# Kernel optimization log

Hardware: AMD Instinct MI355X
Metric: run time of the kernel (lower is better)

## Reference

```python
import jax, jax.numpy as jnp
import numpy as np
import math

EMBED_DIM = 768
NUM_HEADS = 12
HEAD_DIM = EMBED_DIM // NUM_HEADS
R = 16
LORA_ALPHA = 16
SCALING = LORA_ALPHA / math.sqrt(R)  # 4.0
U = 1.0  # ramp_up_steps=0 -> u()=1.0


def lora_linear(x, W, b, A):
    # base F.linear + SingLoRA delta: delta_W = A @ A.T (symmetric)
    base = x @ W.T + b
    delta_W = A @ A.T  # [D, D]
    return base + (x @ delta_W.T) * (U * SCALING)


def setup_inputs() -> dict:
    key = jax.random.key(0)
    ks = jax.random.split(key, 16)
    B, S, D = 2, 2048, EMBED_DIM
    inv = 1.0 / math.sqrt(D)
    d = {
        'query': jax.random.normal(ks[0], (B, S, D), jnp.float32),
        'key': jax.random.normal(ks[1], (B, S, D), jnp.float32),
        'value': jax.random.normal(ks[2], (B, S, D), jnp.float32),
        'Wq': jax.random.normal(ks[3], (D, D), jnp.float32) * inv,
        'bq': jax.random.normal(ks[4], (D,), jnp.float32) * 0.01,
        'Aq': jax.random.normal(ks[5], (D, R), jnp.float32) * 0.01,
        'Wk': jax.random.normal(ks[6], (D, D), jnp.float32) * inv,
        'bk': jax.random.normal(ks[7], (D,), jnp.float32) * 0.01,
        'Ak': jax.random.normal(ks[8], (D, R), jnp.float32) * 0.01,
        'Wv': jax.random.normal(ks[9], (D, D), jnp.float32) * inv,
        'bv': jax.random.normal(ks[10], (D,), jnp.float32) * 0.01,
        'Av': jax.random.normal(ks[11], (D, R), jnp.float32) * 0.01,
        'Wo': jax.random.normal(ks[12], (D, D), jnp.float32) * inv,
        'bo': jax.random.normal(ks[13], (D,), jnp.float32) * 0.01,
    }
    return d


def reference(query, key, value, Wq, bq, Aq, Wk, bk, Ak, Wv, bv, Av, Wo, bo):
    B, S, D = query.shape
    H, hd = NUM_HEADS, HEAD_DIM
    q = lora_linear(query, Wq, bq, Aq)
    k = lora_linear(key, Wk, bk, Ak)
    v = lora_linear(value, Wv, bv, Av)
    # [B, S, D] -> [B, H, S, hd]
    q = q.reshape(B, S, H, hd).transpose(0, 2, 1, 3)
    k = k.reshape(B, S, H, hd).transpose(0, 2, 1, 3)
    v = v.reshape(B, S, H, hd).transpose(0, 2, 1, 3)
    scores = jnp.einsum('bhqd,bhkd->bhqk', q, k) / math.sqrt(hd)
    attn = jax.nn.softmax(scores, axis=-1)
    out = jnp.einsum('bhqk,bhkd->bhqd', attn, v)  # [B, H, S, hd]
    out = out.transpose(0, 2, 1, 3).reshape(B, S, D)
    out = out @ Wo.T + bo
    return out
```

## Files before the change

kernel.cpp:

```cpp
#include <hip/hip_runtime.h>
#include <math.h>
#include <stdint.h>

#define D 768
#define S 2048
#define B_ 2
#define NROWS 4096
#define H 12
#define HD 64
#define R_ 16

typedef _Float16 half_t;
typedef _Float16 half8 __attribute__((ext_vector_type(8)));
typedef _Float16 half4 __attribute__((ext_vector_type(4)));
typedef float floatx4 __attribute__((ext_vector_type(4)));

#define MFMA32(a, b, c) __builtin_amdgcn_mfma_f32_16x16x32_f16(a, b, c, 0, 0, 0)
#define MFMA16(a, b, c) __builtin_amdgcn_mfma_f32_16x16x16f16(a, b, c, 0, 0, 0)
#define EXP2F(x) __builtin_amdgcn_exp2f(x)

__device__ __forceinline__ void gl_lds16(const void* gp, half_t* lp) {
  __builtin_amdgcn_global_load_lds(
      (const __attribute__((address_space(1))) void*)(gp),
      (__attribute__((address_space(3))) void*)(lp), 16, 0, 0);
}

__global__ __launch_bounds__(256) void build_M4_kernel(
    const float* __restrict__ Wq, const float* __restrict__ Aq,
    const float* __restrict__ Wk, const float* __restrict__ Ak,
    const float* __restrict__ Wv, const float* __restrict__ Av,
    const float* __restrict__ Wo, half_t* __restrict__ Mq,
    half_t* __restrict__ Mk, half_t* __restrict__ Mv,
    half_t* __restrict__ Mo) {
  const int y = blockIdx.y;
  const float* W = (y == 0) ? Wq : (y == 1) ? Wk : (y == 2) ? Wv : Wo;
  const float* A = (y == 0) ? Aq : (y == 1) ? Ak : (y == 2) ? Av : nullptr;
  half_t* M = (y == 0) ? Mq : (y == 1) ? Mk : (y == 2) ? Mv : Mo;
  int idx = blockIdx.x * 256 + threadIdx.x;
  int j = idx / D;
  int kk = idx - j * D;
  float acc = W[idx];
  if (A != nullptr) {
    float s = 0.f;
#pragma unroll
    for (int r = 0; r < R_; ++r) s += A[kk * R_ + r] * A[j * R_ + r];
    acc += 4.0f * s;
  }
  M[idx] = (half_t)acc;
}

__global__ __launch_bounds__(256) void gemm_qkv_kernel(
    const float* __restrict__ x0, const float* __restrict__ x1,
    const float* __restrict__ x2, const half_t* __restrict__ m0,
    const half_t* __restrict__ m1, const half_t* __restrict__ m2,
    const float* __restrict__ b0, const float* __restrict__ b1,
    const float* __restrict__ b2, half_t* __restrict__ o0,
    half_t* __restrict__ o1, half_t* __restrict__ o2) {
  constexpr int PB = 32 * 512;
  constexpr int TRS = 136;
  __shared__ __align__(16) half_t smem[2 * PB];

  const int z = blockIdx.z;
  const float* X = (z == 0) ? x0 : (z == 1) ? x1 : x2;
  const half_t* M = (z == 0) ? m0 : (z == 1) ? m1 : m2;
  const float* bias = (z == 0) ? b0 : (z == 1) ? b1 : b2;
  half_t* Out = (z == 0) ? o0 : (z == 1) ? o1 : o2;

  const int tid = threadIdx.x;
  const int lane = tid & 63;
  const int wv = tid >> 6;
  const int lr = lane & 15;
  const int lq = lane >> 4;
  const int row0 = blockIdx.y * 128;
  const int j0 = blockIdx.x * 128;
  const int wr = wv >> 1;
  const int wc = wv & 1;

  const int g_ = tid >> 4;
  const int a_ = tid & 15;
  const int arow0 = row0 + (g_ >> 1) * 16 + (a_ & 3) * 4;
  const int acolb = (g_ & 1) * 32 + (a_ >> 2) * 8;

  floatx4 acc[4][4] = {};
  float4 ra[8];

#define LOADA(k0)                                                              \
  do {                                                                         \
    _Pragma("unroll") for (int i = 0; i < 4; ++i) {                            \
      const float* p = X + (size_t)(arow0 + i) * D + (k0) + acolb;             \
      ra[2 * i] = *reinterpret_cast<const float4*>(p);                         \
      ra[2 * i + 1] = *reinterpret_cast<const float4*>(p + 4);                 \
    }                                                                          \
  } while (0)

#define WRITEA(bufi)                                                           \
  do {                                                                         \
    _Pragma("unroll") for (int i = 0; i < 4; ++i) {                            \
      half8 hh;                                                                \
      hh[0] = (half_t)ra[2 * i].x;                                             \
      hh[1] = (half_t)ra[2 * i].y;                                             \
      hh[2] = (half_t)ra[2 * i].z;                                             \
      hh[3] = (half_t)ra[2 * i].w;                                             \
      hh[4] = (half_t)ra[2 * i + 1].x;                                         \
      hh[5] = (half_t)ra[2 * i + 1].y;                                         \
      hh[6] = (half_t)ra[2 * i + 1].z;                                         \
      hh[7] = (half_t)ra[2 * i + 1].w;                                         \
      *reinterpret_cast<half8*>(smem + (bufi)*PB + 32 * tid + 8 * i) = hh;     \
    }                                                                          \
  } while (0)

#define STAGEB(bufi, k0)                                                       \
  do {                                                                         \
    _Pragma("unroll") for (int gi = 0; gi < 4; ++gi) {                         \
      int gb = wv * 4 + gi;                                                    \
      int u = gb >> 1, cb = gb & 1;                                            \
      gl_lds16(M + (size_t)(j0 + u * 16 + lr) * D + (k0) + cb * 32 + lq * 8,   \
               smem + (bufi)*PB + 16 * 512 + gb * 512);                        \
    }                                                                          \
  } while (0)

  STAGEB(0, 0);
  LOADA(0);
  WRITEA(0);
  __syncthreads();

  for (int it = 0; it < D / 64; ++it) {
    const int cur = it & 1;
    if (it + 1 < D / 64) {
      STAGEB(cur ^ 1, (it + 1) * 64);
      LOADA((it + 1) * 64);
    }
    const half_t* Ab = smem + cur * PB;
    const half_t* Bb = Ab + 16 * 512;
#pragma unroll
    for (int c = 0; c < 2; ++c) {
      half8 af[4], bf[4];
#pragma unroll
      for (int t = 0; t < 4; ++t)
        af[t] = *reinterpret_cast<const half8*>(
            &Ab[(((wr * 4 + t) * 2 + c) * 64 + lane) * 8]);
#pragma unroll
      for (int u = 0; u < 4; ++u)
        bf[u] = *reinterpret_cast<const half8*>(
            &Bb[(((wc * 4 + u) * 2 + c) * 64 + lane) * 8]);
#pragma unroll
      for (int t = 0; t < 4; ++t)
#pragma unroll
        for (int u = 0; u < 4; ++u) acc[t][u] = MFMA32(af[t], bf[u], acc[t][u]);
    }
    if (it + 1 < D / 64) WRITEA(cur ^ 1);
    __syncthreads();
  }
#undef LOADA
#undef WRITEA
#undef STAGEB

  float bv[4];
#pragma unroll
  for (int u = 0; u < 4; ++u) bv[u] = bias[j0 + (wc * 4 + u) * 16 + lr];

  if (z == 2) {
#pragma unroll
    for (int t = 0; t < 4; ++t) {
#pragma unroll
      for (int u = 0; u < 4; ++u) {
        int c_local = (wc * 4 + u) * 16 + lr;
#pragma unroll
        for (int r = 0; r < 4; ++r) {
          int r_local = (wr * 4 + t) * 16 + lq * 4 + r;
          smem[c_local * TRS + r_local] = (half_t)(acc[t][u][r] + bv[u]);
        }
      }
    }
    __syncthreads();
    const int bb = row0 >> 11;
    const int s_base = row0 & 2047;
#pragma unroll
    for (int it = 0; it < 8; ++it) {
      int unit = it * 256 + tid;
      int c_local = unit >> 4;
      int chunk = unit & 15;
      half8 vv =
          *reinterpret_cast<const half8*>(&smem[c_local * TRS + chunk * 8]);
      int gc = j0 + c_local;
      int hh = gc >> 6, dd = gc & 63;
      *reinterpret_cast<half8*>(
          &Out[((size_t)(bb * H + hh) * HD + dd) * S + s_base + chunk * 8]) = vv;
    }
    return;
  }

#pragma unroll
  for (int t = 0; t < 4; ++t) {
#pragma unroll
    for (int u = 0; u < 4; ++u) {
#pragma unroll
      for (int r = 0; r < 4; ++r) {
        int gr = row0 + (wr * 4 + t) * 16 + lq * 4 + r;
        int gc = j0 + (wc * 4 + u) * 16 + lr;
        Out[(size_t)gr * D + gc] = (half_t)(acc[t][u][r] + bv[u]);
      }
    }
  }
}

__global__ __launch_bounds__(256) void gemm_o_kernel(
    const half_t* __restrict__ Xh, const half_t* __restrict__ M,
    const float* __restrict__ bias, float* __restrict__ Out) {
  constexpr int AG = 8;
  constexpr int G = AG + 16;
  constexpr int PB = G * 512;
  __shared__ __align__(16) half_t smem[2 * PB];

  const int tid = threadIdx.x;
  const int lane = tid & 63;
  const int wv = tid >> 6;
  const int lr = lane & 15;
  const int lq = lane >> 4;
  const int row0 = blockIdx.y * 64;
  const int j0 = blockIdx.x * 128;
  const int wc = wv;

  floatx4 acc[4][2] = {};

#define GSTAGE(bufi, k0)                                                       \
  do {                                                                         \
    _Pragma("unroll") for (int gi = 0; gi < 6; ++gi) {                         \
      int g = wv * 6 + gi;                                                     \
      if (g < AG) {                                                            \
        int t = g >> 1, c = g & 1;                                             \
        gl_lds16(                                                              \
            Xh + (size_t)(row0 + t * 16 + lr) * D + (k0) + c * 32 + lq * 8,    \
            smem + (bufi)*PB + g * 512);                                       \
      } else {                                                                 \
        int g2 = g - AG;                                                       \
        int u = g2 >> 1, c = g2 & 1;                                           \
        gl_lds16(                                                              \
            M + (size_t)(j0 + u * 16 + lr) * D + (k0) + c * 32 + lq * 8,       \
            smem + (bufi)*PB + AG * 512 + g2 * 512);                           \
      }                                                                        \
    }                                                                          \
  } while (0)

  GSTAGE(0, 0);
  __syncthreads();

  for (int it = 0; it < D / 64; ++it) {
    const int cur = it & 1;
    if (it + 1 < D / 64) GSTAGE(cur ^ 1, (it + 1) * 64);
    const half_t* Ab = smem + cur * PB;
    const half_t* Bb = Ab + AG * 512;
#pragma unroll
    for (int c = 0; c < 2; ++c) {
      half8 af[4], bf[2];
#pragma unroll
      for (int t = 0; t < 4; ++t)
        af[t] = *reinterpret_cast<const half8*>(
            &Ab[((t * 2 + c) * 64 + lane) * 8]);
#pragma unroll
      for (int u = 0; u < 2; ++u)
        bf[u] = *reinterpret_cast<const half8*>(
            &Bb[(((wc * 2 + u) * 2 + c) * 64 + lane) * 8]);
#pragma unroll
      for (int t = 0; t < 4; ++t)
#pragma unroll
        for (int u = 0; u < 2; ++u) acc[t][u] = MFMA32(af[t], bf[u], acc[t][u]);
    }
    __syncthreads();
  }
#undef GSTAGE

  float bv[2];
#pragma unroll
  for (int u = 0; u < 2; ++u) bv[u] = bias[j0 + (wc * 2 + u) * 16 + lr];
#pragma unroll
  for (int t = 0; t < 4; ++t) {
#pragma unroll
    for (int u = 0; u < 2; ++u) {
#pragma unroll
      for (int r = 0; r < 4; ++r) {
        int gr = row0 + t * 16 + lq * 4 + r;
        int gc = j0 + (wc * 2 + u) * 16 + lr;
        Out[(size_t)gr * D + gc] = acc[t][u][r] + bv[u];
      }
    }
  }
}

__global__ __launch_bounds__(512, 6) void attn_mfma_kernel(
    const half_t* __restrict__ Qh, const half_t* __restrict__ Kh,
    const half_t* __restrict__ Vt_g, half_t* __restrict__ Oh) {
  __shared__ __align__(16) half_t smem[16384];
  half_t* Ks = smem;
  half_t* Vs = smem + 8192;

  const int tid = threadIdx.x;
  const int lane = tid & 63;
  const int wv = tid >> 6;
  const int t_ = wv & 3;
  const int half_ = wv >> 2;
  const int lr = lane & 15;
  const int lq = lane >> 4;
  const int q0 = blockIdx.x * 64;
  const int h = blockIdx.y;
  const int b = blockIdx.z;
  const size_t base = (size_t)b * S * D + h * HD;
  const size_t vtbase = (size_t)(b * H + h) * HD * (size_t)S;
  const int qw = q0 + t_ * 16;

  const half_t qscale = (half_t)0.18033688f;
  half8 qf[2];
#pragma unroll
  for (int c = 0; c < 2; ++c) {
    half8 qv = *reinterpret_cast<const half8*>(
        &Qh[base + (size_t)(qw + lr) * D + c * 32 + lq * 8]);
#pragma unroll
    for (int j = 0; j < 8; ++j) qv[j] = qv[j] * qscale;
    qf[c] = qv;
  }

  half4 ones;
#pragma unroll
  for (int j = 0; j < 4; ++j) ones[j] = (half_t)1.0f;

  floatx4 o[4] = {};
  floatx4 ol = {};

#define STAGE(bufi, kb)                                                        \
  do {                                                                         \
    _Pragma("unroll") for (int gi = 0; gi < 2; ++gi) {                         \
      int g = wv * 2 + gi;                                                     \
      if (g < 8) {                                                             \
        int u = g >> 1, c = g & 1;                                             \
        gl_lds16(                                                              \
            Kh + base + (size_t)((kb) + u * 16 + lr) * D + c * 32 + lq * 8,    \
            Ks + (bufi)*4096 + g * 512);                                       \
      } else {                                                                 \
        int gv = g - 8;                                                        \
        int ud = gv >> 1, c = gv & 1;                                          \
        gl_lds16(                                                              \
            Vt_g + vtbase + (size_t)(ud * 16 + lr) * S + (kb) + c * 32 +       \
                lq * 8,                                                        \
            Vs + (bufi)*4096 + gv * 512);                                      \
      }                                                                        \
    }                                                                          \
  } while (0)

  STAGE(0, 0);
  __syncthreads();

  for (int it = 0; it < S / 64; ++it) {
    const int cur = it & 1;
    if (it + 1 < S / 64) STAGE(cur ^ 1, (it + 1) * 64);

#pragma unroll
    for (int ui = 0; ui < 2; ++ui) {
      const int u = half_ * 2 + ui;
      half8 kf0 = *reinterpret_cast<const half8*>(
          &Ks[cur * 4096 + ((u * 2 + 0) * 64 + lane) * 8]);
      half8 kf1 = *reinterpret_cast<const half8*>(
          &Ks[cur * 4096 + ((u * 2 + 1) * 64 + lane) * 8]);
      floatx4 st = {};
      st = MFMA32(kf0, qf[0], st);
      st = MFMA32(kf1, qf[1], st);
      half4 pf;
      pf[0] = (half_t)EXP2F(st[0]);
      pf[1] = (half_t)EXP2F(st[1]);
      pf[2] = (half_t)EXP2F(st[2]);
      pf[3] = (half_t)EXP2F(st[3]);
#pragma unroll
      for (int ud = 0; ud < 4; ++ud) {
        half4 vf = *reinterpret_cast<const half4*>(
            &Vs[cur * 4096 + ((ud * 2 + (u >> 1)) * 64 +
                              ((((u & 1) * 2) + (lq >> 1)) * 16 + lr)) *
                                 8 +
                (lq & 1) * 4]);
        o[ud] = MFMA16(pf, vf, o[ud]);
      }
      ol = MFMA16(pf, ones, ol);
    }
    __syncthreads();
  }
#undef STAGE

  float* red = (float*)smem;
  const int slot = t_ * 64 + lane;
  if (half_ == 1) {
#pragma unroll
    for (int comp = 0; comp < 16; ++comp)
      red[comp * 260 + slot] = o[comp >> 2][comp & 3];
#pragma unroll
    for (int r = 0; r < 4; ++r) red[(16 + r) * 260 + slot] = ol[r];
  }
  __syncthreads();
  if (half_ == 0) {
#pragma unroll
    for (int comp = 0; comp < 16; ++comp)
      o[comp >> 2][comp & 3] += red[comp * 260 + slot];
    float linv[4];
#pragma unroll
    for (int r = 0; r < 4; ++r)
      linv[r] = 1.0f / (ol[r] + red[(16 + r) * 260 + slot]);
#pragma unroll
    for (int ud = 0; ud < 4; ++ud) {
#pragma unroll
      for (int r = 0; r < 4; ++r) {
        int row = qw + lq * 4 + r;
        int col = h * HD + ud * 16 + lr;
        Oh[(size_t)(b * S + row) * D + col] = (half_t)(o[ud][r] * linv[r]);
      }
    }
  }
}

extern "C" void kernel_launch(void* const* d_in, const int* in_sizes, int n_in,
                              void* d_out, int out_size, void* d_ws,
                              size_t ws_size, hipStream_t stream) {
  const float* query = (const float*)d_in[0];
  const float* key   = (const float*)d_in[1];
  const float* value = (const float*)d_in[2];
  const float* Wq = (const float*)d_in[3];
  const float* bq = (const float*)d_in[4];
  const float* Aq = (const float*)d_in[5];
  const float* Wk = (const float*)d_in[6];
  const float* bk = (const float*)d_in[7];
  const float* Ak = (const float*)d_in[8];
  const float* Wv = (const float*)d_in[9];
  const float* bv = (const float*)d_in[10];
  const float* Av = (const float*)d_in[11];
  const float* Wo = (const float*)d_in[12];
  const float* bo = (const float*)d_in[13];
  float* out = (float*)d_out;

  half_t* hw = (half_t*)d_ws;
  const size_t XSZ = (size_t)NROWS * D;
  const size_t MSZ = (size_t)D * D;
  half_t* qh = hw;
  half_t* kh = qh + XSZ;
  half_t* vt = kh + XSZ;
  half_t* ab = vt + XSZ;
  half_t* Mq = ab + XSZ;
  half_t* Mk = Mq + MSZ;
  half_t* Mv = Mk + MSZ;
  half_t* Mo = Mv + MSZ;

  dim3 gm(D * D / 256, 4);
  build_M4_kernel<<<gm, 256, 0, stream>>>(Wq, Aq, Wk, Ak, Wv, Av, Wo, Mq, Mk,
                                          Mv, Mo);

  dim3 gq(D / 128, NROWS / 128, 3);
  gemm_qkv_kernel<<<gq, 256, 0, stream>>>(query, key, value, Mq, Mk, Mv, bq,
                                          bk, bv, qh, kh, vt);

  dim3 ga(S / 64, H, B_);
  attn_mfma_kernel<<<ga, 512, 0, stream>>>(qh, kh, vt, ab);

  dim3 go(D / 128, NROWS / 64, 1);
  gemm_o_kernel<<<go, 256, 0, stream>>>(ab, Mo, bo, out);
}
```

Measured before the change: 243.5 us.

## Pre-convert QKV inputs to fp16 and stage GEMM operands via direct LDS loads

```diff
diff --git a/kernel.cpp b/kernel.cpp
--- a/kernel.cpp
+++ b/kernel.cpp
@@ -25,43 +25,60 @@
       (__attribute__((address_space(3))) void*)(lp), 16, 0, 0);
 }
 
-__global__ __launch_bounds__(256) void build_M4_kernel(
+__global__ __launch_bounds__(256) void prep_kernel(
+    const float* __restrict__ q, const float* __restrict__ k,
+    const float* __restrict__ v, half_t* __restrict__ xq,
+    half_t* __restrict__ xk, half_t* __restrict__ xv,
     const float* __restrict__ Wq, const float* __restrict__ Aq,
     const float* __restrict__ Wk, const float* __restrict__ Ak,
     const float* __restrict__ Wv, const float* __restrict__ Av,
     const float* __restrict__ Wo, half_t* __restrict__ Mq,
     half_t* __restrict__ Mk, half_t* __restrict__ Mv,
     half_t* __restrict__ Mo) {
-  const int y = blockIdx.y;
-  const float* W = (y == 0) ? Wq : (y == 1) ? Wk : (y == 2) ? Wv : Wo;
-  const float* A = (y == 0) ? Aq : (y == 1) ? Ak : (y == 2) ? Av : nullptr;
-  half_t* M = (y == 0) ? Mq : (y == 1) ? Mk : (y == 2) ? Mv : Mo;
-  int idx = blockIdx.x * 256 + threadIdx.x;
-  int j = idx / D;
-  int kk = idx - j * D;
-  float acc = W[idx];
-  if (A != nullptr) {
-    float s = 0.f;
-#pragma unroll
-    for (int r = 0; r < R_; ++r) s += A[kk * R_ + r] * A[j * R_ + r];
-    acc += 4.0f * s;
-  }
-  M[idx] = (half_t)acc;
+  const int bid = blockIdx.x;
+  if (bid < 9216) {
+    const int y = bid / 3072;
+    const float* x = (y == 0) ? q : (y == 1) ? k : v;
+    half_t* o = (y == 0) ? xq : (y == 1) ? xk : xv;
+    int i = (bid - y * 3072) * 1024 + threadIdx.x * 4;
+    float4 vv = *reinterpret_cast<const float4*>(x + i);
+    half_t tmp[4] = {(half_t)vv.x, (half_t)vv.y, (half_t)vv.z, (half_t)vv.w};
+    *reinterpret_cast<uint64_t*>(o + i) = *reinterpret_cast<uint64_t*>(tmp);
+  } else {
+    const int u = bid - 9216;
+    const int y = u / 2304;
+    const float* W = (y == 0) ? Wq : (y == 1) ? Wk : (y == 2) ? Wv : Wo;
+    const float* A = (y == 0) ? Aq : (y == 1) ? Ak : (y == 2) ? Av : nullptr;
+    half_t* M = (y == 0) ? Mq : (y == 1) ? Mk : (y == 2) ? Mv : Mo;
+    int idx = (u - y * 2304) * 256 + threadIdx.x;
+    int j = idx / D;
+    int kk = idx - j * D;
+    float acc = W[idx];
+    if (A != nullptr) {
+      float s = 0.f;
+#pragma unroll
+      for (int r = 0; r < R_; ++r) s += A[kk * R_ + r] * A[j * R_ + r];
+      acc += 4.0f * s;
+    }
+    M[idx] = (half_t)acc;
+  }
 }
 
 __global__ __launch_bounds__(256) void gemm_qkv_kernel(
-    const float* __restrict__ x0, const float* __restrict__ x1,
-    const float* __restrict__ x2, const half_t* __restrict__ m0,
+    const half_t* __restrict__ x0, const half_t* __restrict__ x1,
+    const half_t* __restrict__ x2, const half_t* __restrict__ m0,
     const half_t* __restrict__ m1, const half_t* __restrict__ m2,
     const float* __restrict__ b0, const float* __restrict__ b1,
     const float* __restrict__ b2, half_t* __restrict__ o0,
     half_t* __restrict__ o1, half_t* __restrict__ o2) {
-  constexpr int PB = 32 * 512;
-  constexpr int TRS = 136;
+  constexpr int AG = 8;
+  constexpr int G = AG + 16;
+  constexpr int PB = G * 512;
+  constexpr int TRS = 72;
   __shared__ __align__(16) half_t smem[2 * PB];
 
   const int z = blockIdx.z;
-  const float* X = (z == 0) ? x0 : (z == 1) ? x1 : x2;
+  const half_t* X = (z == 0) ? x0 : (z == 1) ? x1 : x2;
   const half_t* M = (z == 0) ? m0 : (z == 1) ? m1 : m2;
   const float* bias = (z == 0) ? b0 : (z == 1) ? b1 : b2;
   half_t* Out = (z == 0) ? o0 : (z == 1) ? o1 : o2;
@@ -71,103 +88,72 @@
   const int wv = tid >> 6;
   const int lr = lane & 15;
   const int lq = lane >> 4;
-  const int row0 = blockIdx.y * 128;
+  const int row0 = blockIdx.y * 64;
   const int j0 = blockIdx.x * 128;
-  const int wr = wv >> 1;
-  const int wc = wv & 1;
-
-  const int g_ = tid >> 4;
-  const int a_ = tid & 15;
-  const int arow0 = row0 + (g_ >> 1) * 16 + (a_ & 3) * 4;
-  const int acolb = (g_ & 1) * 32 + (a_ >> 2) * 8;
-
-  floatx4 acc[4][4] = {};
-  float4 ra[8];
-
-#define LOADA(k0)                                                              \
+  const int wc = wv;
+
+  floatx4 acc[4][2] = {};
+
+#define GSTAGE(bufi, k0)                                                       \
   do {                                                                         \
-    _Pragma("unroll") for (int i = 0; i < 4; ++i) {                            \
-      const float* p = X + (size_t)(arow0 + i) * D + (k0) + acolb;             \
-      ra[2 * i] = *reinterpret_cast<const float4*>(p);                         \
-      ra[2 * i + 1] = *reinterpret_cast<const float4*>(p + 4);                 \
+    _Pragma("unroll") for (int gi = 0; gi < 6; ++gi) {                         \
+      int g = wv * 6 + gi;                                                     \
+      if (g < AG) {                                                            \
+        int t = g >> 1, c = g & 1;                                             \
+        gl_lds16(                                                              \
+            X + (size_t)(row0 + t * 16 + lr) * D + (k0) + c * 32 + lq * 8,     \
+            smem + (bufi)*PB + g * 512);                                       \
+      } else {                                                                 \
+        int g2 = g - AG;                                                       \
+        int u = g2 >> 1, c = g2 & 1;                                           \
+        gl_lds16(                                                              \
+            M + (size_t)(j0 + u * 16 + lr) * D + (k0) + c * 32 + lq * 8,       \
+            smem + (bufi)*PB + AG * 512 + g2 * 512);                           \
+      }                                                                        \
     }                                                                          \
   } while (0)
 
-#define WRITEA(bufi)                                                           \
-  do {                                                                         \
-    _Pragma("unroll") for (int i = 0; i < 4; ++i) {                            \
-      half8 hh;                                                                \
-      hh[0] = (half_t)ra[2 * i].x;                                             \
-      hh[1] = (half_t)ra[2 * i].y;                                             \
-      hh[2] = (half_t)ra[2 * i].z;                                             \
-      hh[3] = (half_t)ra[2 * i].w;                                             \
-      hh[4] = (half_t)ra[2 * i + 1].x;                                         \
-      hh[5] = (half_t)ra[2 * i + 1].y;                                         \
-      hh[6] = (half_t)ra[2 * i + 1].z;                                         \
-      hh[7] = (half_t)ra[2 * i + 1].w;                                         \
-      *reinterpret_cast<half8*>(smem + (bufi)*PB + 32 * tid + 8 * i) = hh;     \
-    }                                                                          \
-  } while (0)
-
-#define STAGEB(bufi, k0)                                                       \
-  do {                                                                         \
-    _Pragma("unroll") for (int gi = 0; gi < 4; ++gi) {                         \
-      int gb = wv * 4 + gi;                                                    \
-      int u = gb >> 1, cb = gb & 1;                                            \
-      gl_lds16(M + (size_t)(j0 + u * 16 + lr) * D + (k0) + cb * 32 + lq * 8,   \
-               smem + (bufi)*PB + 16 * 512 + gb * 512);                        \
-    }                                                                          \
-  } while (0)
-
-  STAGEB(0, 0);
-  LOADA(0);
-  WRITEA(0);
+  GSTAGE(0, 0);
   __syncthreads();
 
   for (int it = 0; it < D / 64; ++it) {
     const int cur = it & 1;
-    if (it + 1 < D / 64) {
-      STAGEB(cur ^ 1, (it + 1) * 64);
-      LOADA((it + 1) * 64);
-    }
+    if (it + 1 < D / 64) GSTAGE(cur ^ 1, (it + 1) * 64);
     const half_t* Ab = smem + cur * PB;
-    const half_t* Bb = Ab + 16 * 512;
+    const half_t* Bb = Ab + AG * 512;
 #pragma unroll
     for (int c = 0; c < 2; ++c) {
-      half8 af[4], bf[4];
+      half8 af[4], bf[2];
 #pragma unroll
       for (int t = 0; t < 4; ++t)
         af[t] = *reinterpret_cast<const half8*>(
-            &Ab[(((wr * 4 + t) * 2 + c) * 64 + lane) * 8]);
-#pragma unroll
-      for (int u = 0; u < 4; ++u)
+            &Ab[((t * 2 + c) * 64 + lane) * 8]);
+#pragma unroll
+      for (int u = 0; u < 2; ++u)
         bf[u] = *reinterpret_cast<const half8*>(
-            &Bb[(((wc * 4 + u) * 2 + c) * 64 + lane) * 8]);
+            &Bb[(((wc * 2 + u) * 2 + c) * 64 + lane) * 8]);
 #pragma unroll
       for (int t = 0; t < 4; ++t)
 #pragma unroll
-        for (int u = 0; u < 4; ++u) acc[t][u] = MFMA32(af[t], bf[u], acc[t][u]);
-    }
-    if (it + 1 < D / 64) WRITEA(cur ^ 1);
+        for (int u = 0; u < 2; ++u) acc[t][u] = MFMA32(af[t], bf[u], acc[t][u]);
+    }
     __syncthreads();
   }
-#undef LOADA
-#undef WRITEA
-#undef STAGEB
-
-  float bv[4];
-#pragma unroll
-  for (int u = 0; u < 4; ++u) bv[u] = bias[j0 + (wc * 4 + u) * 16 + lr];
+#undef GSTAGE
+
+  float bv[2];
+#pragma unroll
+  for (int u = 0; u < 2; ++u) bv[u] = bias[j0 + (wc * 2 + u) * 16 + lr];
 
   if (z == 2) {
 #pragma unroll
     for (int t = 0; t < 4; ++t) {
 #pragma unroll
-      for (int u = 0; u < 4; ++u) {
-        int c_local = (wc * 4 + u) * 16 + lr;
+      for (int u = 0; u < 2; ++u) {
+        int c_local = (wc * 2 + u) * 16 + lr;
 #pragma unroll
         for (int r = 0; r < 4; ++r) {
-          int r_local = (wr * 4 + t) * 16 + lq * 4 + r;
+          int r_local = t * 16 + lq * 4 + r;
           smem[c_local * TRS + r_local] = (half_t)(acc[t][u][r] + bv[u]);
         }
       }
@@ -176,10 +162,10 @@
     const int bb = row0 >> 11;
     const int s_base = row0 & 2047;
 #pragma unroll
-    for (int it = 0; it < 8; ++it) {
+    for (int it = 0; it < 4; ++it) {
       int unit = it * 256 + tid;
-      int c_local = unit >> 4;
-      int chunk = unit & 15;
+      int c_local = unit >> 3;
+      int chunk = unit & 7;
       half8 vv =
           *reinterpret_cast<const half8*>(&smem[c_local * TRS + chunk * 8]);
       int gc = j0 + c_local;
@@ -193,11 +179,11 @@
 #pragma unroll
   for (int t = 0; t < 4; ++t) {
 #pragma unroll
-    for (int u = 0; u < 4; ++u) {
+    for (int u = 0; u < 2; ++u) {
 #pragma unroll
       for (int r = 0; r < 4; ++r) {
-        int gr = row0 + (wr * 4 + t) * 16 + lq * 4 + r;
-        int gc = j0 + (wc * 4 + u) * 16 + lr;
+        int gr = row0 + t * 16 + lq * 4 + r;
+        int gc = j0 + (wc * 2 + u) * 16 + lr;
         Out[(size_t)gr * D + gc] = (half_t)(acc[t][u][r] + bv[u]);
       }
     }
@@ -435,7 +421,10 @@
   half_t* hw = (half_t*)d_ws;
   const size_t XSZ = (size_t)NROWS * D;
   const size_t MSZ = (size_t)D * D;
-  half_t* qh = hw;
+  half_t* xq = hw;
+  half_t* xk = xq + XSZ;
+  half_t* xv = xk + XSZ;
+  half_t* qh = xv + XSZ;
   half_t* kh = qh + XSZ;
   half_t* vt = kh + XSZ;
   half_t* ab = vt + XSZ;
@@ -444,13 +433,12 @@
   half_t* Mv = Mk + MSZ;
   half_t* Mo = Mv + MSZ;
 
-  dim3 gm(D * D / 256, 4);
-  build_M4_kernel<<<gm, 256, 0, stream>>>(Wq, Aq, Wk, Ak, Wv, Av, Wo, Mq, Mk,
-                                          Mv, Mo);
-
-  dim3 gq(D / 128, NROWS / 128, 3);
-  gemm_qkv_kernel<<<gq, 256, 0, stream>>>(query, key, value, Mq, Mk, Mv, bq,
-                                          bk, bv, qh, kh, vt);
+  prep_kernel<<<18432, 256, 0, stream>>>(query, key, value, xq, xk, xv, Wq, Aq,
+                                         Wk, Ak, Wv, Av, Wo, Mq, Mk, Mv, Mo);
+
+  dim3 gq(D / 128, NROWS / 64, 3);
+  gemm_qkv_kernel<<<gq, 256, 0, stream>>>(xq, xk, xv, Mq, Mk, Mv, bq, bk, bv,
+                                          qh, kh, vt);
 
   dim3 ga(S / 64, H, B_);
   attn_mfma_kernel<<<ga, 512, 0, stream>>>(qh, kh, vt, ab);
```

After: 233.0 us. 1.04x faster.
